# Kernel tuning notes

Measured on AMD Instinct MI355X. Metric: run time of the kernel, lower is better.

The kernel has to match this reference:

```python
import jax, jax.numpy as jnp
import numpy as np

EPS = 1e-12  # torch F.normalize default eps

def _l2norm(x, axis=-1):
    n = jnp.sqrt(jnp.sum(x * x, axis=axis, keepdims=True))
    return x / jnp.maximum(n, EPS)

def setup_inputs() -> dict:
    key = jax.random.key(0)
    k1, k2, k3 = jax.random.split(key, 3)
    B, L, D, C, J = 16, 1024, 768, 500, 10
    spatial = jax.random.normal(k1, (B, L, D), dtype=jnp.float32)
    prototypes = jax.random.normal(k2, (C, J, D), dtype=jnp.float32) * 0.02
    raw_weights = jnp.full((C, J), -2.0, dtype=jnp.float32) + 0.1 * jax.random.normal(k3, (C, J), dtype=jnp.float32)
    bias = jnp.zeros((C,), dtype=jnp.float32)
    return {"spatial": spatial, "prototypes": prototypes, "raw_weights": raw_weights, "bias": bias}

def reference(spatial, prototypes, raw_weights, bias):
    # spatial: (B, L, D); prototypes: (C, J, D)
    z = _l2norm(spatial)            # (B, L, D)
    p = _l2norm(prototypes)         # (C, J, D)
    sim = jnp.einsum('bld,cjd->blcj', z, p)   # (B, L, C, J)
    pooled = jnp.max(sim, axis=1)              # (B, C, J) max over L
    weights = jax.nn.softplus(raw_weights)     # (C, J)
    logits = jnp.sum(pooled * weights[None], axis=-1) + bias  # (B, C)
    return logits
```

## Files before the change

### kernel.cpp

```cpp
#include <hip/hip_runtime.h>

#define B_     16
#define L_     1024
#define D_     768
#define C_     500
#define J_     10
#define M_     (B_ * L_)
#define NREAL  (C_ * J_)
#define NPAD   5120
#define TM     256
#define TN     256
#define TK     64
#define KTILES (D_ / TK)

typedef __attribute__((ext_vector_type(8))) short short8;
typedef __attribute__((ext_vector_type(4))) float f32x4;

struct frag2 { short8 k[2]; };

static __device__ __forceinline__ unsigned f2ord(float f) {
    unsigned u = __float_as_uint(f);
    return (u & 0x80000000u) ? ~u : (u | 0x80000000u);
}
static __device__ __forceinline__ float ord2f(unsigned u) {
    return (u & 0x80000000u) ? __uint_as_float(u & 0x7fffffffu)
                             : __uint_as_float(~u);
}

static __device__ __forceinline__ unsigned short f2bf(float f) {
    unsigned u = __float_as_uint(f);
    u += 0x7fffu + ((u >> 16) & 1u);
    return (unsigned short)(u >> 16);
}

__global__ __launch_bounds__(256) void norm_rows_kernel(
    const float* __restrict__ in, unsigned short* __restrict__ out,
    int nrows, int valid_rows)
{
    int row  = blockIdx.x * 4 + (threadIdx.x >> 6);
    int lane = threadIdx.x & 63;
    if (row >= nrows) return;

    unsigned short* orow = out + (size_t)row * D_;
    if (row >= valid_rows) {
        ushort4 z = {0, 0, 0, 0};
        #pragma unroll
        for (int p = 0; p < 3; ++p)
            *(ushort4*)(orow + (p * 64 + lane) * 4) = z;
        return;
    }

    const float4* rp = (const float4*)(in + (size_t)row * D_);
    float4 v[3];
    float s = 0.f;
    #pragma unroll
    for (int p = 0; p < 3; ++p) {
        v[p] = rp[p * 64 + lane];
        s += v[p].x * v[p].x + v[p].y * v[p].y + v[p].z * v[p].z + v[p].w * v[p].w;
    }
    #pragma unroll
    for (int off = 32; off; off >>= 1) s += __shfl_xor(s, off);
    float inv = 1.f / fmaxf(sqrtf(s), 1e-12f);
    #pragma unroll
    for (int p = 0; p < 3; ++p) {
        ushort4 o;
        o.x = f2bf(v[p].x * inv);
        o.y = f2bf(v[p].y * inv);
        o.z = f2bf(v[p].z * inv);
        o.w = f2bf(v[p].w * inv);
        *(ushort4*)(orow + (p * 64 + lane) * 4) = o;
    }
}


#define MFMA(a, b, c) __builtin_amdgcn_mfma_f32_16x16x32_bf16(a, b, c, 0, 0, 0)
#define FENCE asm volatile("" ::: "memory")
#define BAR   do { FENCE; __builtin_amdgcn_s_barrier(); FENCE; } while (0)
#define VM(N) asm volatile("s_waitcnt vmcnt(" #N ")" ::: "memory")
#define PRIO1 __builtin_amdgcn_s_setprio(1)
#define PRIO0 __builtin_amdgcn_s_setprio(0)

#define RD_A2(dst, p, mi) do { \
    dst[0].k[0] = *(const short8*)(bA0 + (p)*32768 + (mi)*1024); \
    dst[0].k[1] = *(const short8*)(bA1 + (p)*32768 + (mi)*1024); \
    dst[1].k[0] = *(const short8*)(bA0 + (p)*32768 + ((mi)+1)*1024); \
    dst[1].k[1] = *(const short8*)(bA1 + (p)*32768 + ((mi)+1)*1024); \
} while (0)

#define RD_B4(dst, p) do { \
    _Pragma("unroll") \
    for (int ni_ = 0; ni_ < 4; ++ni_) { \
        dst[ni_].k[0] = *(const short8*)(bB0 + (p)*32768 + ni_*1024); \
        dst[ni_].k[1] = *(const short8*)(bB1 + (p)*32768 + ni_*1024); \
    } \
} while (0)

#define STAGE_A(p, q, k0) __builtin_amdgcn_global_load_lds( \
    (const __attribute__((address_space(1))) void*)(Z + gA0 + (q)*64*D_ + (unsigned)(k0)), \
    (__attribute__((address_space(3))) void*)(lds + (p)*32768 + (q)*4096 + tid8), 16, 0, 0)
#define STAGE_B(p, q, k0) __builtin_amdgcn_global_load_lds( \
    (const __attribute__((address_space(1))) void*)(Pm + gB0 + (q)*64*D_ + (unsigned)(k0)), \
    (__attribute__((address_space(3))) void*)(lds + (p)*32768 + 16384 + (q)*4096 + tid8), 16, 0, 0)

#define MMPAIR(j, S, Bv) do { \
    PRIO1; \
    _Pragma("unroll") \
    for (int ni_ = 0; ni_ < 4; ++ni_) { \
        acc[2*(j)][ni_]   = MFMA(S[0].k[0], Bv[ni_].k[0], acc[2*(j)][ni_]); \
        acc[2*(j)+1][ni_] = MFMA(S[1].k[0], Bv[ni_].k[0], acc[2*(j)+1][ni_]); \
        acc[2*(j)][ni_]   = MFMA(S[0].k[1], Bv[ni_].k[1], acc[2*(j)][ni_]); \
        acc[2*(j)+1][ni_] = MFMA(S[1].k[1], Bv[ni_].k[1], acc[2*(j)+1][ni_]); \
    } \
    PRIO0; \
} while (0)

__global__ __launch_bounds__(512, 1) void gemm_maxpool_kernel(
    const unsigned short* __restrict__ Z,
    const unsigned short* __restrict__ Pm,
    unsigned int* __restrict__ pooled)
{
    __shared__ unsigned short lds[65536];

    const int tid  = threadIdx.x;
    const int lane = tid & 63;
    const int wid  = tid >> 6;
    const int wm   = wid >> 2;
    const int wn   = wid & 3;

    const int xcd = (int)blockIdx.x & 7;
    const int idx = (int)blockIdx.x >> 3;
    const int bm  = xcd * 8 + (idx & 7);
    const int bn  = idx >> 3;
    const int row0 = bm * TM;
    const int col0 = bn * TN;

    const int tr    = tid >> 3;
    const int tswz  = ((tid & 7) * 16) ^ ((tr & 7) << 4);
    const int tid8  = tid * 8;
    const unsigned gA0 = (unsigned)(row0 + tr) * D_ + (tswz >> 1);
    const unsigned gB0 = (unsigned)(col0 + tr) * D_ + (tswz >> 1);

    const int l15   = lane & 15;
    const int swzl  = (lane & 7) << 4;
    const int colS0 = ((((lane >> 4) * 16)      ) ^ swzl) >> 1;
    const int colS1 = ((((lane >> 4) * 16) + 64 ) ^ swzl) >> 1;
    const unsigned short* bA0 = lds + (wm * 128 + l15) * 64 + colS0;
    const unsigned short* bA1 = lds + (wm * 128 + l15) * 64 + colS1;
    const unsigned short* bB0 = lds + 16384 + (wn * 64 + l15) * 64 + colS0;
    const unsigned short* bB1 = lds + 16384 + (wn * 64 + l15) * 64 + colS1;

    f32x4 acc[8][4] = {};
    frag2 aE[2], aO[2], bE[4], bO[4];

    STAGE_B(0,0,0);  STAGE_B(0,1,0);  STAGE_A(0,0,0);  STAGE_A(0,2,0);
    STAGE_B(0,2,0);  STAGE_B(0,3,0);  STAGE_A(0,1,0);  STAGE_A(0,3,0);
    STAGE_B(1,0,64); STAGE_B(1,1,64); STAGE_A(1,0,64); STAGE_A(1,2,64);
    STAGE_B(1,2,64); STAGE_B(1,3,64); STAGE_A(1,1,64); STAGE_A(1,3,64);
    VM(8);
    BAR;
    RD_B4(bE, 0);
    RD_A2(aE, 0, 0);

    #pragma unroll 1
    for (int i = 0; i < 5; ++i) {
        const int kE = i * 128 + 128;
        const int kO = i * 128 + 192;
        frag2 t23[2], t45[2], t67[2];

        RD_A2(t23, 0, 2);  STAGE_B(0, 0, kE);  STAGE_B(0, 1, kE);
        BAR; MMPAIR(0, aE, bE); BAR;

        RD_A2(t45, 0, 4);  STAGE_A(0, 0, kE);  STAGE_A(0, 2, kE);
        BAR; MMPAIR(1, t23, bE); BAR;

        RD_A2(t67, 0, 6);  STAGE_B(0, 2, kE);  STAGE_B(0, 3, kE);
        VM(6);
        BAR; MMPAIR(2, t45, bE); BAR;

        STAGE_A(0, 1, kE);  STAGE_A(0, 3, kE);
        MMPAIR(3, t67, bE);
        RD_B4(bO, 1);  RD_A2(aO, 1, 0);
        BAR;

        RD_A2(t23, 1, 2);  STAGE_B(1, 0, kO);  STAGE_B(1, 1, kO);
        BAR; MMPAIR(0, aO, bO); BAR;

        RD_A2(t45, 1, 4);  STAGE_A(1, 0, kO);  STAGE_A(1, 2, kO);
        BAR; MMPAIR(1, t23, bO); BAR;

        RD_A2(t67, 1, 6);  STAGE_B(1, 2, kO);  STAGE_B(1, 3, kO);
        VM(6);
        BAR; MMPAIR(2, t45, bO); BAR;

        STAGE_A(1, 1, kO);  STAGE_A(1, 3, kO);
        MMPAIR(3, t67, bO);
        RD_B4(bE, 0);  RD_A2(aE, 0, 0);
        BAR;
    }

    {
        frag2 t23[2], t45[2], t67[2];
        RD_A2(t23, 0, 2);
        BAR; MMPAIR(0, aE, bE); BAR;
        RD_A2(t45, 0, 4);
        BAR; MMPAIR(1, t23, bE); BAR;
        RD_A2(t67, 0, 6);
        VM(0);
        BAR; MMPAIR(2, t45, bE); BAR;
        MMPAIR(3, t67, bE);
        RD_B4(bO, 1);  RD_A2(aO, 1, 0);
        BAR;

        RD_A2(t23, 1, 2);
        BAR; MMPAIR(0, aO, bO); BAR;
        RD_A2(t45, 1, 4);
        BAR; MMPAIR(1, t23, bO); BAR;
        RD_A2(t67, 1, 6);
        BAR; MMPAIR(2, t45, bO); BAR;
        MMPAIR(3, t67, bO);
    }

    const int batch = row0 >> 10;
    #pragma unroll
    for (int ni = 0; ni < 4; ++ni) {
        float v = -3.0e38f;
        #pragma unroll
        for (int mi = 0; mi < 8; ++mi)
            v = fmaxf(v, fmaxf(fmaxf(acc[mi][ni][0], acc[mi][ni][1]),
                               fmaxf(acc[mi][ni][2], acc[mi][ni][3])));
        v = fmaxf(v, __shfl_xor(v, 16));
        v = fmaxf(v, __shfl_xor(v, 32));
        if (lane < 16) {
            int col = col0 + wn * 64 + ni * 16 + lane;
            atomicMax(&pooled[(size_t)batch * NPAD + col], f2ord(v));
        }
    }
}

__global__ __launch_bounds__(256) void finalize_kernel(
    const unsigned int* __restrict__ pooled,
    const float* __restrict__ rw,
    const float* __restrict__ bias,
    float* __restrict__ out)
{
    int t = blockIdx.x * 256 + threadIdx.x;
    if (t >= B_ * C_) return;
    int b = t / C_, c = t % C_;
    float s = 0.f;
    #pragma unroll
    for (int j = 0; j < J_; ++j) {
        float pv = ord2f(pooled[(size_t)b * NPAD + c * J_ + j]);
        float x  = rw[c * J_ + j];
        float w  = fmaxf(x, 0.f) + log1pf(expf(-fabsf(x)));
        s += pv * w;
    }
    out[t] = s + bias[c];
}

extern "C" void kernel_launch(void* const* d_in, const int* in_sizes, int n_in,
                              void* d_out, int out_size, void* d_ws, size_t ws_size,
                              hipStream_t stream) {
    const float* spatial = (const float*)d_in[0];
    const float* protos  = (const float*)d_in[1];
    const float* rw      = (const float*)d_in[2];
    const float* bias    = (const float*)d_in[3];
    float* out = (float*)d_out;

    unsigned short* z = (unsigned short*)d_ws;
    unsigned short* p = z + (size_t)M_ * D_;
    unsigned int* pooled = (unsigned int*)(p + (size_t)NPAD * D_);

    norm_rows_kernel<<<M_ / 4, 256, 0, stream>>>(spatial, z, M_, M_);
    norm_rows_kernel<<<NPAD / 4, 256, 0, stream>>>(protos, p, NPAD, NREAL);
    hipMemsetAsync(pooled, 0, (size_t)B_ * NPAD * sizeof(unsigned int), stream);
    gemm_maxpool_kernel<<<(M_ / TM) * (NPAD / TN), 512, 0, stream>>>(z, p, pooled);
    finalize_kernel<<<(B_ * C_ + 255) / 256, 256, 0, stream>>>(pooled, rw, bias, out);
}
```

Before: 122.0 us.

## Make GEMM persistent over column tiles and fuse prep kernels

Merges the two normalization launches and the pooled-buffer memset into one prep kernel. The GEMM now launches 256 blocks, one per CU, and each block walks 5 consecutive 256-column tiles. The software pipeline runs continuously across tile boundaries by prefetching the next tile's first K-slices during the last iteration of the current one. This removes the per-tile prologue and epilogue pipeline bubbles and the wave-quantization tail of 1280 blocks, at the cost of a fixed schedule and atomics issued mid-loop.

```diff
diff --git a/kernel.cpp b/kernel.cpp
--- a/kernel.cpp
+++ b/kernel.cpp
@@ -12,6 +12,7 @@
 #define TN     256
 #define TK     64
 #define KTILES (D_ / TK)
+#define DCOL   ((unsigned)TN * D_)
 
 typedef __attribute__((ext_vector_type(8))) short short8;
 typedef __attribute__((ext_vector_type(4))) float f32x4;
@@ -33,20 +34,30 @@
     return (unsigned short)(u >> 16);
 }
 
-__global__ __launch_bounds__(256) void norm_rows_kernel(
-    const float* __restrict__ in, unsigned short* __restrict__ out,
-    int nrows, int valid_rows)
+__global__ __launch_bounds__(256) void prep_kernel(
+    const float* __restrict__ spatial, const float* __restrict__ protos,
+    unsigned short* __restrict__ z, unsigned short* __restrict__ pbuf,
+    unsigned int* __restrict__ pooled)
 {
-    int row  = blockIdx.x * 4 + (threadIdx.x >> 6);
-    int lane = threadIdx.x & 63;
-    if (row >= nrows) return;
+    const int bid = blockIdx.x;
+    if (bid < 80) {
+        uint4 zz = {0, 0, 0, 0};
+        *(uint4*)(pooled + bid * 1024 + threadIdx.x * 4) = zz;
+    }
+
+    const float* in;
+    unsigned short* out;
+    int row, valid;
+    if (bid < 4096) { in = spatial; out = z;    row = bid * 4 + (threadIdx.x >> 6);          valid = M_; }
+    else            { in = protos;  out = pbuf; row = (bid - 4096) * 4 + (threadIdx.x >> 6); valid = NREAL; }
+    const int lane = threadIdx.x & 63;
 
     unsigned short* orow = out + (size_t)row * D_;
-    if (row >= valid_rows) {
-        ushort4 z = {0, 0, 0, 0};
+    if (row >= valid) {
+        ushort4 zz = {0, 0, 0, 0};
         #pragma unroll
         for (int p = 0; p < 3; ++p)
-            *(ushort4*)(orow + (p * 64 + lane) * 4) = z;
+            *(ushort4*)(orow + (p * 64 + lane) * 4) = zz;
         return;
     }
 
@@ -98,8 +109,8 @@
 #define STAGE_A(p, q, k0) __builtin_amdgcn_global_load_lds( \
     (const __attribute__((address_space(1))) void*)(Z + gA0 + (q)*64*D_ + (unsigned)(k0)), \
     (__attribute__((address_space(3))) void*)(lds + (p)*32768 + (q)*4096 + tid8), 16, 0, 0)
-#define STAGE_B(p, q, k0) __builtin_amdgcn_global_load_lds( \
-    (const __attribute__((address_space(1))) void*)(Pm + gB0 + (q)*64*D_ + (unsigned)(k0)), \
+#define STAGE_B(p, q, k0, GB) __builtin_amdgcn_global_load_lds( \
+    (const __attribute__((address_space(1))) void*)(Pm + (GB) + (q)*64*D_ + (unsigned)(k0)), \
     (__attribute__((address_space(3))) void*)(lds + (p)*32768 + 16384 + (q)*4096 + tid8), 16, 0, 0)
 
 #define MMPAIR(j, S, Bv) do { \
@@ -128,17 +139,17 @@
     const int wn   = wid & 3;
 
     const int xcd = (int)blockIdx.x & 7;
-    const int idx = (int)blockIdx.x >> 3;
-    const int bm  = xcd * 8 + (idx & 7);
-    const int bn  = idx >> 3;
+    const int lb  = (int)blockIdx.x >> 3;
+    const int bm  = xcd * 8 + (lb & 7);
+    const int bng = lb >> 3;
     const int row0 = bm * TM;
-    const int col0 = bn * TN;
+    int col0 = bng * 5 * TN;
 
     const int tr    = tid >> 3;
     const int tswz  = ((tid & 7) * 16) ^ ((tr & 7) << 4);
     const int tid8  = tid * 8;
     const unsigned gA0 = (unsigned)(row0 + tr) * D_ + (tswz >> 1);
-    const unsigned gB0 = (unsigned)(col0 + tr) * D_ + (tswz >> 1);
+    unsigned gBc = (unsigned)(col0 + tr) * D_ + (tswz >> 1);
 
     const int l15   = lane & 15;
     const int swzl  = (lane & 7) << 4;
@@ -152,89 +163,84 @@
     f32x4 acc[8][4] = {};
     frag2 aE[2], aO[2], bE[4], bO[4];
 
-    STAGE_B(0,0,0);  STAGE_B(0,1,0);  STAGE_A(0,0,0);  STAGE_A(0,2,0);
-    STAGE_B(0,2,0);  STAGE_B(0,3,0);  STAGE_A(0,1,0);  STAGE_A(0,3,0);
-    STAGE_B(1,0,64); STAGE_B(1,1,64); STAGE_A(1,0,64); STAGE_A(1,2,64);
-    STAGE_B(1,2,64); STAGE_B(1,3,64); STAGE_A(1,1,64); STAGE_A(1,3,64);
+    STAGE_B(0,0,0,gBc);  STAGE_B(0,1,0,gBc);  STAGE_A(0,0,0);  STAGE_A(0,2,0);
+    STAGE_B(0,2,0,gBc);  STAGE_B(0,3,0,gBc);  STAGE_A(0,1,0);  STAGE_A(0,3,0);
+    STAGE_B(1,0,64,gBc); STAGE_B(1,1,64,gBc); STAGE_A(1,0,64); STAGE_A(1,2,64);
+    STAGE_B(1,2,64,gBc); STAGE_B(1,3,64,gBc); STAGE_A(1,1,64); STAGE_A(1,3,64);
     VM(8);
     BAR;
     RD_B4(bE, 0);
     RD_A2(aE, 0, 0);
 
     #pragma unroll 1
-    for (int i = 0; i < 5; ++i) {
-        const int kE = i * 128 + 128;
-        const int kO = i * 128 + 192;
-        frag2 t23[2], t45[2], t67[2];
-
-        RD_A2(t23, 0, 2);  STAGE_B(0, 0, kE);  STAGE_B(0, 1, kE);
-        BAR; MMPAIR(0, aE, bE); BAR;
-
-        RD_A2(t45, 0, 4);  STAGE_A(0, 0, kE);  STAGE_A(0, 2, kE);
-        BAR; MMPAIR(1, t23, bE); BAR;
-
-        RD_A2(t67, 0, 6);  STAGE_B(0, 2, kE);  STAGE_B(0, 3, kE);
-        VM(6);
-        BAR; MMPAIR(2, t45, bE); BAR;
-
-        STAGE_A(0, 1, kE);  STAGE_A(0, 3, kE);
-        MMPAIR(3, t67, bE);
-        RD_B4(bO, 1);  RD_A2(aO, 1, 0);
-        BAR;
-
-        RD_A2(t23, 1, 2);  STAGE_B(1, 0, kO);  STAGE_B(1, 1, kO);
-        BAR; MMPAIR(0, aO, bO); BAR;
-
-        RD_A2(t45, 1, 4);  STAGE_A(1, 0, kO);  STAGE_A(1, 2, kO);
-        BAR; MMPAIR(1, t23, bO); BAR;
-
-        RD_A2(t67, 1, 6);  STAGE_B(1, 2, kO);  STAGE_B(1, 3, kO);
-        VM(6);
-        BAR; MMPAIR(2, t45, bO); BAR;
-
-        STAGE_A(1, 1, kO);  STAGE_A(1, 3, kO);
-        MMPAIR(3, t67, bO);
-        RD_B4(bE, 0);  RD_A2(aE, 0, 0);
-        BAR;
-    }
-
-    {
-        frag2 t23[2], t45[2], t67[2];
-        RD_A2(t23, 0, 2);
-        BAR; MMPAIR(0, aE, bE); BAR;
-        RD_A2(t45, 0, 4);
-        BAR; MMPAIR(1, t23, bE); BAR;
-        RD_A2(t67, 0, 6);
-        VM(0);
-        BAR; MMPAIR(2, t45, bE); BAR;
-        MMPAIR(3, t67, bE);
-        RD_B4(bO, 1);  RD_A2(aO, 1, 0);
-        BAR;
-
-        RD_A2(t23, 1, 2);
-        BAR; MMPAIR(0, aO, bO); BAR;
-        RD_A2(t45, 1, 4);
-        BAR; MMPAIR(1, t23, bO); BAR;
-        RD_A2(t67, 1, 6);
-        BAR; MMPAIR(2, t45, bO); BAR;
-        MMPAIR(3, t67, bO);
-    }
-
-    const int batch = row0 >> 10;
-    #pragma unroll
-    for (int ni = 0; ni < 4; ++ni) {
-        float v = -3.0e38f;
+    for (int t = 0; t < 5; ++t) {
+        const unsigned gBn = (t < 4) ? gBc + DCOL : gBc;
+
+        #pragma unroll 1
+        for (int i = 0; i < 6; ++i) {
+            const int wrap = (i == 5);
+            const unsigned bB = wrap ? gBn : gBc;
+            const unsigned kE = wrap ? 0u  : (unsigned)(i * 128 + 128);
+            const unsigned kO = wrap ? 64u : (unsigned)(i * 128 + 192);
+            frag2 t23[2], t45[2], t67[2];
+
+            RD_A2(t23, 0, 2);  STAGE_B(0, 0, kE, bB);  STAGE_B(0, 1, kE, bB);
+            BAR; MMPAIR(0, aE, bE); BAR;
+
+            RD_A2(t45, 0, 4);  STAGE_A(0, 0, kE);  STAGE_A(0, 2, kE);
+            BAR; MMPAIR(1, t23, bE); BAR;
+
+            RD_A2(t67, 0, 6);  STAGE_B(0, 2, kE, bB);  STAGE_B(0, 3, kE, bB);
+            VM(6);
+            BAR; MMPAIR(2, t45, bE); BAR;
+
+            STAGE_A(0, 1, kE);  STAGE_A(0, 3, kE);
+            MMPAIR(3, t67, bE);
+            RD_B4(bO, 1);  RD_A2(aO, 1, 0);
+            BAR;
+
+            RD_A2(t23, 1, 2);  STAGE_B(1, 0, kO, bB);  STAGE_B(1, 1, kO, bB);
+            BAR; MMPAIR(0, aO, bO); BAR;
+
+            RD_A2(t45, 1, 4);  STAGE_A(1, 0, kO);  STAGE_A(1, 2, kO);
+            BAR; MMPAIR(1, t23, bO); BAR;
+
+            RD_A2(t67, 1, 6);  STAGE_B(1, 2, kO, bB);  STAGE_B(1, 3, kO, bB);
+            VM(6);
+            BAR; MMPAIR(2, t45, bO); BAR;
+
+            STAGE_A(1, 1, kO);  STAGE_A(1, 3, kO);
+            MMPAIR(3, t67, bO);
+            RD_B4(bE, 0);  RD_A2(aE, 0, 0);
+            BAR;
+        }
+
+        const int batch = row0 >> 10;
+        #pragma unroll
+        for (int ni = 0; ni < 4; ++ni) {
+            float v = -3.0e38f;
+            #pragma unroll
+            for (int mi = 0; mi < 8; ++mi)
+                v = fmaxf(v, fmaxf(fmaxf(acc[mi][ni][0], acc[mi][ni][1]),
+                                   fmaxf(acc[mi][ni][2], acc[mi][ni][3])));
+            v = fmaxf(v, __shfl_xor(v, 16));
+            v = fmaxf(v, __shfl_xor(v, 32));
+            if (lane < 16) {
+                int col = col0 + wn * 64 + ni * 16 + lane;
+                atomicMax(&pooled[(size_t)batch * NPAD + col], f2ord(v));
+            }
+        }
         #pragma unroll
         for (int mi = 0; mi < 8; ++mi)
-            v = fmaxf(v, fmaxf(fmaxf(acc[mi][ni][0], acc[mi][ni][1]),
-                               fmaxf(acc[mi][ni][2], acc[mi][ni][3])));
-        v = fmaxf(v, __shfl_xor(v, 16));
-        v = fmaxf(v, __shfl_xor(v, 32));
-        if (lane < 16) {
-            int col = col0 + wn * 64 + ni * 16 + lane;
-            atomicMax(&pooled[(size_t)batch * NPAD + col], f2ord(v));
-        }
-    }
+            #pragma unroll
+            for (int ni = 0; ni < 4; ++ni)
+                acc[mi][ni] = (f32x4){0.f, 0.f, 0.f, 0.f};
+
+        gBc = gBn;
+        col0 += TN;
+    }
+
+    VM(0);
 }
 
 __global__ __launch_bounds__(256) void finalize_kernel(
@@ -270,9 +276,7 @@
     unsigned short* p = z + (size_t)M_ * D_;
     unsigned int* pooled = (unsigned int*)(p + (size_t)NPAD * D_);
 
-    norm_rows_kernel<<<M_ / 4, 256, 0, stream>>>(spatial, z, M_, M_);
-    norm_rows_kernel<<<NPAD / 4, 256, 0, stream>>>(protos, p, NPAD, NREAL);
-    hipMemsetAsync(pooled, 0, (size_t)B_ * NPAD * sizeof(unsigned int), stream);
-    gemm_maxpool_kernel<<<(M_ / TM) * (NPAD / TN), 512, 0, stream>>>(z, p, pooled);
+    prep_kernel<<<M_ / 4 + NPAD / 4, 256, 0, stream>>>(spatial, protos, z, p, pooled);
+    gemm_maxpool_kernel<<<256, 512, 0, stream>>>(z, p, pooled);
     finalize_kernel<<<(B_ * C_ + 255) / 256, 256, 0, stream>>>(pooled, rw, bias, out);
 }
```

Measured after the change: 125.1 us. 1.03x slower.
